# Kernel optimization log

Hardware: AMD Instinct MI355X
Metric: run time of the kernel (lower is better)

The kernel has to match this reference:

```python
import jax, jax.numpy as jnp
import numpy as np

BITS = 4
MAXQ = (1 << BITS) - 1  # 15
GROUPSIZE = 128
IN_F = 8192
OUT_F = 8192
PACK = 32 // BITS  # 8 values per int32


def setup_inputs() -> dict:
    key = jax.random.key(0)
    k_x, k_w, k_z, k_s, k_b = jax.random.split(key, 5)
    groups = IN_F // GROUPSIZE
    x = jax.random.normal(k_x, (4, 32, IN_F), dtype=jnp.float32)
    # bit-packed int32 weight / zeros (random bit patterns are valid quantized data)
    qweight = jax.random.randint(k_w, (IN_F // PACK, OUT_F), 0, 2**31 - 1, dtype=jnp.int32)
    qzeros = jax.random.randint(k_z, (groups, OUT_F // PACK), 0, 2**31 - 1, dtype=jnp.int32)
    scales = (jax.random.uniform(k_s, (groups, OUT_F), dtype=jnp.float32) * 0.01 + 1e-3)
    g_idx = (jnp.arange(IN_F, dtype=jnp.int32) // GROUPSIZE).astype(jnp.int32)
    bias = jax.random.normal(k_b, (OUT_F,), dtype=jnp.float32) * 0.01
    return {"x": x, "qweight": qweight, "qzeros": qzeros, "scales": scales,
            "g_idx": g_idx, "bias": bias}


def _dequant(qweight, qzeros, scales, g_idx):
    shifts = jnp.arange(0, 32, BITS, dtype=jnp.int32)  # [PACK]
    # unpack weights along the input dim: [in/PACK, PACK, out] -> [in, out]
    w = (qweight[:, None, :] >> shifts[None, :, None]) & MAXQ
    w = w.reshape(-1, qweight.shape[1])
    # unpack zeros along the output dim: [groups, out/PACK, PACK] -> [groups, out]
    # GPTQ stores (zero - 1), so add 1 back
    z = ((qzeros[:, :, None] >> shifts[None, None, :]) & MAXQ) + 1
    z = z.reshape(qzeros.shape[0], -1)
    # per-group dequant: W[i, o] = scales[g_idx[i], o] * (w[i, o] - z[g_idx[i], o])
    W = scales[g_idx] * (w.astype(scales.dtype) - z[g_idx].astype(scales.dtype))
    return W  # [in, out]


def reference(x, qweight, qzeros, scales, g_idx, bias):
    W = _dequant(qweight, qzeros, scales, g_idx)
    out = jnp.einsum('bsi,io->bso', x, W) + bias
    return out
```

## Files before the change

kernel.cpp:

```cpp
#include <hip/hip_runtime.h>
#include <hip/hip_bf16.h>
#include <stdint.h>


#define IN_F 8192
#define OUT_F 8192
#define MROWS 128
#define KSPLIT 8
#define KCHUNK 1024
#define BM 64

typedef short short8_t __attribute__((ext_vector_type(8)));
typedef float float4_t __attribute__((ext_vector_type(4)));
typedef float float16_t __attribute__((ext_vector_type(16)));

__global__ void reduce_out(const float* __restrict__ part, const float* __restrict__ bias,
                           float* __restrict__ out) {
  const int i = (blockIdx.x * 256 + threadIdx.x) * 4;
  const int o = i & (OUT_F - 1);
  float4_t s = *(const float4_t*)(bias + o);
#pragma unroll
  for (int sl = 0; sl < KSPLIT; ++sl)
    s += *(const float4_t*)(part + (size_t)sl * MROWS * OUT_F + i);
  *(float4_t*)(out + i) = s;
}

__global__ __launch_bounds__(512, 2) void gptq_gemm(
    const float* __restrict__ x,
    const int* __restrict__ qweight,
    const int* __restrict__ qzeros,
    const float* __restrict__ scales,
    float* __restrict__ part)
{
  __shared__ unsigned short As[BM * KCHUNK];

  const int tid  = threadIdx.x;
  const int lane = tid & 63;
  const int l31  = lane & 31;
  const int half = lane >> 5;
  const int wv   = tid >> 6;

  const int bid = blockIdx.x;
  const int kb  = bid >> 5;
  const int mb  = (bid >> 4) & 1;
  const int nb  = bid & 15;

  const int kc0 = kb * KCHUNK;
  const int m0  = mb * BM;
  const int g0  = kc0 >> 7;
  const int kp_base = (kc0 >> 3) + half;

  int col[2];
  col[0] = nb * 512 + wv * 64 + l31;
  col[1] = col[0] + 32;

  int   qw[3][8][2];
  float sc[3][2];
  int   zq[3][2];

  auto prefetch = [&](int gg, int buf) {
    const int kp = kp_base + gg * 16;
#pragma unroll
    for (int ks = 0; ks < 8; ++ks)
#pragma unroll
      for (int nt = 0; nt < 2; ++nt)
        qw[buf][ks][nt] = qweight[(size_t)(kp + ks * 2) * OUT_F + col[nt]];
    const int gg_abs = g0 + gg;
#pragma unroll
    for (int nt = 0; nt < 2; ++nt) {
      sc[buf][nt] = scales[gg_abs * OUT_F + col[nt]];
      zq[buf][nt] = qzeros[gg_abs * (OUT_F / 8) + (col[nt] >> 3)];
    }
  };

  prefetch(0, 0);
  prefetch(1, 1);

  for (int rq = 0; rq < 8; ++rq) {
    const int rl = wv * 8 + rq;
    const float* grow = x + (size_t)(m0 + rl) * IN_F + kc0;
#pragma unroll
    for (int hf = 0; hf < 2; ++hf) {
      const int p = hf * 64 + lane;
      const int c = (p & 0x70) | ((p ^ (rl & 15)) & 15);
      float4_t a = *(const float4_t*)(grow + c * 8);
      float4_t b = *(const float4_t*)(grow + c * 8 + 4);
      union { short8_t v; __hip_bfloat162 h[4]; } u;
      u.h[0] = __float22bfloat162_rn(make_float2(a.x, a.y));
      u.h[1] = __float22bfloat162_rn(make_float2(a.z, a.w));
      u.h[2] = __float22bfloat162_rn(make_float2(b.x, b.y));
      u.h[3] = __float22bfloat162_rn(make_float2(b.z, b.w));
      *(short8_t*)(As + ((size_t)rl * 128 + p) * 8) = u.v;
    }
  }
  __syncthreads();

  float16_t acc[2][2];
#pragma unroll
  for (int mt = 0; mt < 2; ++mt)
#pragma unroll
    for (int nt = 0; nt < 2; ++nt)
#pragma unroll
      for (int r = 0; r < 16; ++r) acc[mt][nt][r] = 0.f;

#pragma unroll
  for (int g = 0; g < 8; ++g) {
    const int cur = g % 3;

    if (g + 2 < 8) prefetch(g + 2, (g + 2) % 3);

    float zb[2];
#pragma unroll
    for (int nt = 0; nt < 2; ++nt) {
      const int z = ((zq[cur][nt] >> (4 * (col[nt] & 7))) & 15) + 1;
      zb[nt] = -sc[cur][nt] * (float)z;
    }

#pragma unroll
    for (int ks = 0; ks < 8; ++ks) {
      const int c = g * 16 + ks * 2 + half;
      const int p = (c & 0x70) | ((c ^ (l31 & 15)) & 15);

      short8_t af[2];
#pragma unroll
      for (int mt = 0; mt < 2; ++mt)
        af[mt] = *(const short8_t*)(As + ((size_t)(mt * 32 + l31) * 128 + p) * 8);

      short8_t bf[2];
#pragma unroll
      for (int nt = 0; nt < 2; ++nt) {
        union { short8_t v; __hip_bfloat162 h[4]; } bw;
        const unsigned q  = (unsigned)qw[cur][ks][nt];
        const unsigned qe = q & 0x0F0F0F0Fu;
        const unsigned qo = (q >> 4) & 0x0F0F0F0Fu;
#pragma unroll
        for (int jj = 0; jj < 4; ++jj) {
          const float f0 = (float)((qe >> (8 * jj)) & 0xffu);
          const float f1 = (float)((qo >> (8 * jj)) & 0xffu);
          bw.h[jj] = __float22bfloat162_rn(make_float2(
              fmaf(sc[cur][nt], f0, zb[nt]), fmaf(sc[cur][nt], f1, zb[nt])));
        }
        bf[nt] = bw.v;
      }

#pragma unroll
      for (int mt = 0; mt < 2; ++mt)
#pragma unroll
        for (int nt = 0; nt < 2; ++nt)
          acc[mt][nt] = __builtin_amdgcn_mfma_f32_32x32x16_bf16(
              af[mt], bf[nt], acc[mt][nt], 0, 0, 0);
    }
  }

  float* base = part + (size_t)kb * (MROWS * OUT_F);
#pragma unroll
  for (int mt = 0; mt < 2; ++mt)
#pragma unroll
    for (int nt = 0; nt < 2; ++nt)
#pragma unroll
      for (int r = 0; r < 16; ++r) {
        const int row = (r & 3) + 8 * (r >> 2) + 4 * half;
        base[(size_t)(m0 + mt * 32 + row) * OUT_F + col[nt]] = acc[mt][nt][r];
      }
}

extern "C" void kernel_launch(void* const* d_in, const int* in_sizes, int n_in,
                              void* d_out, int out_size, void* d_ws, size_t ws_size,
                              hipStream_t stream) {
  const float* x        = (const float*)d_in[0];
  const int*   qweight  = (const int*)d_in[1];
  const int*   qzeros   = (const int*)d_in[2];
  const float* scales   = (const float*)d_in[3];
  const float* bias     = (const float*)d_in[5];
  float* out = (float*)d_out;

  float* part = (float*)d_ws;

  gptq_gemm<<<dim3(256), 512, 0, stream>>>(x, qweight, qzeros, scales, part);
  reduce_out<<<dim3((MROWS * OUT_F) / (256 * 4)), 256, 0, stream>>>(part, bias, out);
}
```

Baseline: 116.5 us.

## Factor scale and zero out of the MFMA loop using per-group activation row sums

Raw 4-bit weights are now fed to the MFMA as bf16 built directly from the integer-to-float bit patterns, with no per-element scale/zero FMA and rounding. Each group accumulates into a partial accumulator. After each group the partial result is scaled by the column scale, and the zero term is applied via precomputed per-row, per-group sums of the bf16 activations held in shared memory. This takes most of the ALU dequant work out of the inner loop, at the cost of an extra shared-memory row-sum pass, a second barrier and 64 extra accumulator registers, which may hurt occupancy.

```diff
diff --git a/kernel.cpp b/kernel.cpp
--- a/kernel.cpp
+++ b/kernel.cpp
@@ -33,6 +33,7 @@
     float* __restrict__ part)
 {
   __shared__ unsigned short As[BM * KCHUNK];
+  __shared__ float Ss[BM * 8];
 
   const int tid  = threadIdx.x;
   const int lane = tid & 63;
@@ -95,6 +96,24 @@
   }
   __syncthreads();
 
+  {
+    const int row = tid >> 3;
+    const int g   = tid & 7;
+    float s = 0.f;
+#pragma unroll
+    for (int j = 0; j < 16; ++j) {
+      const int c = g * 16 + j;
+      const int p = (c & 0x70) | ((c ^ (row & 15)) & 15);
+      union { short8_t v; unsigned short us[8]; } a;
+      a.v = *(const short8_t*)(As + ((size_t)row * 128 + p) * 8);
+#pragma unroll
+      for (int e = 0; e < 8; ++e)
+        s += __uint_as_float((unsigned)a.us[e] << 16);
+    }
+    Ss[row * 8 + g] = s;
+  }
+  __syncthreads();
+
   float16_t acc[2][2];
 #pragma unroll
   for (int mt = 0; mt < 2; ++mt)
@@ -102,6 +121,8 @@
     for (int nt = 0; nt < 2; ++nt)
 #pragma unroll
       for (int r = 0; r < 16; ++r) acc[mt][nt][r] = 0.f;
+
+  const float16_t zv = (float16_t)0.0f;
 
 #pragma unroll
   for (int g = 0; g < 8; ++g) {
@@ -109,12 +130,7 @@
 
     if (g + 2 < 8) prefetch(g + 2, (g + 2) % 3);
 
-    float zb[2];
-#pragma unroll
-    for (int nt = 0; nt < 2; ++nt) {
-      const int z = ((zq[cur][nt] >> (4 * (col[nt] & 7))) & 15) + 1;
-      zb[nt] = -sc[cur][nt] * (float)z;
-    }
+    float16_t pacc[2][2];
 
 #pragma unroll
     for (int ks = 0; ks < 8; ++ks) {
@@ -129,7 +145,7 @@
       short8_t bf[2];
 #pragma unroll
       for (int nt = 0; nt < 2; ++nt) {
-        union { short8_t v; __hip_bfloat162 h[4]; } bw;
+        union { short8_t v; unsigned u[4]; } bw;
         const unsigned q  = (unsigned)qw[cur][ks][nt];
         const unsigned qe = q & 0x0F0F0F0Fu;
         const unsigned qo = (q >> 4) & 0x0F0F0F0Fu;
@@ -137,8 +153,8 @@
         for (int jj = 0; jj < 4; ++jj) {
           const float f0 = (float)((qe >> (8 * jj)) & 0xffu);
           const float f1 = (float)((qo >> (8 * jj)) & 0xffu);
-          bw.h[jj] = __float22bfloat162_rn(make_float2(
-              fmaf(sc[cur][nt], f0, zb[nt]), fmaf(sc[cur][nt], f1, zb[nt])));
+          bw.u[jj] = __builtin_amdgcn_perm(__float_as_uint(f1), __float_as_uint(f0),
+                                           0x07060302u);
         }
         bf[nt] = bw.v;
       }
@@ -147,9 +163,28 @@
       for (int mt = 0; mt < 2; ++mt)
 #pragma unroll
         for (int nt = 0; nt < 2; ++nt)
-          acc[mt][nt] = __builtin_amdgcn_mfma_f32_32x32x16_bf16(
-              af[mt], bf[nt], acc[mt][nt], 0, 0, 0);
-    }
+          pacc[mt][nt] = __builtin_amdgcn_mfma_f32_32x32x16_bf16(
+              af[mt], bf[nt], (ks == 0) ? zv : pacc[mt][nt], 0, 0, 0);
+    }
+
+    float c1[2], c2[2];
+#pragma unroll
+    for (int nt = 0; nt < 2; ++nt) {
+      const int z = ((zq[cur][nt] >> (4 * (col[nt] & 7))) & 15) + 1;
+      c1[nt] = sc[cur][nt];
+      c2[nt] = -sc[cur][nt] * (float)z;
+    }
+#pragma unroll
+    for (int mt = 0; mt < 2; ++mt)
+#pragma unroll
+      for (int r = 0; r < 16; ++r) {
+        const int rowr = (r & 3) + 8 * (r >> 2) + 4 * half;
+        const float s = Ss[(mt * 32 + rowr) * 8 + g];
+#pragma unroll
+        for (int nt = 0; nt < 2; ++nt)
+          acc[mt][nt][r] = fmaf(c1[nt], pacc[mt][nt][r],
+                                fmaf(c2[nt], s, acc[mt][nt][r]));
+      }
   }
 
   float* base = part + (size_t)kb * (MROWS * OUT_F);
```

New measurement: 315.1 us. 2.7x slower.

## Split N tile across 16 waves and convert bf16 by truncation via perm

Applied to the files above, without the earlier changes.

Doubles the block to 1024 threads, with each wave owning one 32-column N tile instead of two. This halves per-wave registers and raises the number of resident waves. The bf16 conversion of dequantized weights now truncates with a byte permute instead of round-to-nearest, which cuts ALU work but changes rounding. A-fragment reuse per LDS read is halved.

```diff
diff --git a/kernel.cpp b/kernel.cpp
--- a/kernel.cpp
+++ b/kernel.cpp
@@ -25,7 +25,7 @@
   *(float4_t*)(out + i) = s;
 }
 
-__global__ __launch_bounds__(512, 2) void gptq_gemm(
+__global__ __launch_bounds__(1024, 4) void gptq_gemm(
     const float* __restrict__ x,
     const int* __restrict__ qweight,
     const int* __restrict__ qzeros,
@@ -50,34 +50,27 @@
   const int g0  = kc0 >> 7;
   const int kp_base = (kc0 >> 3) + half;
 
-  int col[2];
-  col[0] = nb * 512 + wv * 64 + l31;
-  col[1] = col[0] + 32;
+  const int col = nb * 512 + wv * 32 + l31;
 
-  int   qw[3][8][2];
-  float sc[3][2];
-  int   zq[3][2];
+  int   qw[3][8];
+  float sc[3];
+  int   zq[3];
 
   auto prefetch = [&](int gg, int buf) {
     const int kp = kp_base + gg * 16;
 #pragma unroll
     for (int ks = 0; ks < 8; ++ks)
-#pragma unroll
-      for (int nt = 0; nt < 2; ++nt)
-        qw[buf][ks][nt] = qweight[(size_t)(kp + ks * 2) * OUT_F + col[nt]];
+      qw[buf][ks] = qweight[(size_t)(kp + ks * 2) * OUT_F + col];
     const int gg_abs = g0 + gg;
-#pragma unroll
-    for (int nt = 0; nt < 2; ++nt) {
-      sc[buf][nt] = scales[gg_abs * OUT_F + col[nt]];
-      zq[buf][nt] = qzeros[gg_abs * (OUT_F / 8) + (col[nt] >> 3)];
-    }
+    sc[buf] = scales[gg_abs * OUT_F + col];
+    zq[buf] = qzeros[gg_abs * (OUT_F / 8) + (col >> 3)];
   };
 
   prefetch(0, 0);
   prefetch(1, 1);
 
-  for (int rq = 0; rq < 8; ++rq) {
-    const int rl = wv * 8 + rq;
+  for (int rq = 0; rq < 4; ++rq) {
+    const int rl = wv * 4 + rq;
     const float* grow = x + (size_t)(m0 + rl) * IN_F + kc0;
 #pragma unroll
     for (int hf = 0; hf < 2; ++hf) {
@@ -95,13 +88,11 @@
   }
   __syncthreads();
 
-  float16_t acc[2][2];
+  float16_t acc[2];
 #pragma unroll
   for (int mt = 0; mt < 2; ++mt)
 #pragma unroll
-    for (int nt = 0; nt < 2; ++nt)
-#pragma unroll
-      for (int r = 0; r < 16; ++r) acc[mt][nt][r] = 0.f;
+    for (int r = 0; r < 16; ++r) acc[mt][r] = 0.f;
 
 #pragma unroll
   for (int g = 0; g < 8; ++g) {
@@ -109,12 +100,9 @@
 
     if (g + 2 < 8) prefetch(g + 2, (g + 2) % 3);
 
-    float zb[2];
-#pragma unroll
-    for (int nt = 0; nt < 2; ++nt) {
-      const int z = ((zq[cur][nt] >> (4 * (col[nt] & 7))) & 15) + 1;
-      zb[nt] = -sc[cur][nt] * (float)z;
-    }
+    const int z = ((zq[cur] >> (4 * (col & 7))) & 15) + 1;
+    const float zb = -sc[cur] * (float)z;
+    const float s = sc[cur];
 
 #pragma unroll
     for (int ks = 0; ks < 8; ++ks) {
@@ -126,29 +114,21 @@
       for (int mt = 0; mt < 2; ++mt)
         af[mt] = *(const short8_t*)(As + ((size_t)(mt * 32 + l31) * 128 + p) * 8);
 
-      short8_t bf[2];
+      union { short8_t v; unsigned u[4]; } bw;
+      const unsigned q  = (unsigned)qw[cur][ks];
+      const unsigned qe = q & 0x0F0F0F0Fu;
+      const unsigned qo = (q >> 4) & 0x0F0F0F0Fu;
 #pragma unroll
-      for (int nt = 0; nt < 2; ++nt) {
-        union { short8_t v; __hip_bfloat162 h[4]; } bw;
-        const unsigned q  = (unsigned)qw[cur][ks][nt];
-        const unsigned qe = q & 0x0F0F0F0Fu;
-        const unsigned qo = (q >> 4) & 0x0F0F0F0Fu;
-#pragma unroll
-        for (int jj = 0; jj < 4; ++jj) {
-          const float f0 = (float)((qe >> (8 * jj)) & 0xffu);
-          const float f1 = (float)((qo >> (8 * jj)) & 0xffu);
-          bw.h[jj] = __float22bfloat162_rn(make_float2(
-              fmaf(sc[cur][nt], f0, zb[nt]), fmaf(sc[cur][nt], f1, zb[nt])));
-        }
-        bf[nt] = bw.v;
+      for (int jj = 0; jj < 4; ++jj) {
+        const float f0 = fmaf(s, (float)((qe >> (8 * jj)) & 0xffu), zb);
+        const float f1 = fmaf(s, (float)((qo >> (8 * jj)) & 0xffu), zb);
+        bw.u[jj] = __builtin_amdgcn_perm(__float_as_uint(f1), __float_as_uint(f0),
+                                         0x07060302u);
       }
 
 #pragma unroll
       for (int mt = 0; mt < 2; ++mt)
-#pragma unroll
-        for (int nt = 0; nt < 2; ++nt)
-          acc[mt][nt] = __builtin_amdgcn_mfma_f32_32x32x16_bf16(
-              af[mt], bf[nt], acc[mt][nt], 0, 0, 0);
+        acc[mt] = __builtin_amdgcn_mfma_f32_32x32x16_bf16(af[mt], bw.v, acc[mt], 0, 0, 0);
     }
   }
 
@@ -156,12 +136,10 @@
 #pragma unroll
   for (int mt = 0; mt < 2; ++mt)
 #pragma unroll
-    for (int nt = 0; nt < 2; ++nt)
-#pragma unroll
-      for (int r = 0; r < 16; ++r) {
-        const int row = (r & 3) + 8 * (r >> 2) + 4 * half;
-        base[(size_t)(m0 + mt * 32 + row) * OUT_F + col[nt]] = acc[mt][nt][r];
-      }
+    for (int r = 0; r < 16; ++r) {
+      const int row = (r & 3) + 8 * (r >> 2) + 4 * half;
+      base[(size_t)(m0 + mt * 32 + row) * OUT_F + col] = acc[mt][r];
+    }
 }
 
 extern "C" void kernel_launch(void* const* d_in, const int* in_sizes, int n_in,
@@ -176,6 +154,6 @@
 
   float* part = (float*)d_ws;
 
-  gptq_gemm<<<dim3(256), 512, 0, stream>>>(x, qweight, qzeros, scales, part);
+  gptq_gemm<<<dim3(256), 1024, 0, stream>>>(x, qweight, qzeros, scales, part);
   reduce_out<<<dim3((MROWS * OUT_F) / (256 * 4)), 256, 0, stream>>>(part, bias, out);
 }
```

Measured after the change: 115.8 us. Within noise of the previous version (-0.6%).
